# Performance work log

Hardware: AMD Instinct MI355X
Metric: run time of the kernel (lower is better)

## Reference

```python
import jax, jax.numpy as jnp
import numpy as np

K = 3          # kernel size (implied by 18/27 offset channels)
PAD = 1
STRIDE = 1


def setup_inputs() -> dict:
    key = jax.random.key(0)
    k0, k1, k2 = jax.random.split(key, 3)
    B, C, H, W = 4, 256, 64, 64
    Cout = 256
    x = jax.random.normal(k0, (B, C, H, W), jnp.float32)
    # offset/mask predicting conv: 18 offset + 9 mask channels (deform_group=1)
    w_off = jax.random.normal(k1, (27, C, K, K), jnp.float32) * 0.01
    b_off = jnp.zeros((27,), jnp.float32)
    # main deformable conv weight (bias=False)
    w = jax.random.normal(k2, (Cout, C, K, K), jnp.float32) * 0.05
    return {"x": x, "w_off": w_off, "b_off": b_off, "w": w}


def _modulated_dcn(x, w_off, b_off, w):
    B, C, H, W = x.shape
    KK = K * K
    # regular conv predicting offsets (+ mask)
    om = jax.lax.conv_general_dilated(
        x, w_off, (STRIDE, STRIDE), [(PAD, PAD), (PAD, PAD)],
        dimension_numbers=("NCHW", "OIHW", "NCHW")) + b_off[None, :, None, None]
    Ho, Wo = om.shape[2], om.shape[3]
    # channel layout: interleaved (dy, dx) per kernel tap, then 9 mask channels
    off = om[:, :2 * KK].reshape(B, KK, 2, Ho, Wo)
    mask = jax.nn.sigmoid(om[:, 2 * KK:3 * KK])            # (B, KK, Ho, Wo)

    ky, kx = jnp.meshgrid(jnp.arange(K), jnp.arange(K), indexing="ij")
    base_y = (jnp.arange(Ho) * STRIDE - PAD)[:, None]       # (Ho, 1)
    base_x = (jnp.arange(Wo) * STRIDE - PAD)[None, :]       # (1, Wo)
    # sampling positions p = p0 + pn + offset, shape (B, KK, Ho, Wo)
    py = base_y[None, None] + ky.reshape(KK)[None, :, None, None] + off[:, :, 0]
    px = base_x[None, None] + kx.reshape(KK)[None, :, None, None] + off[:, :, 1]

    y0f = jnp.floor(py)
    x0f = jnp.floor(px)
    ly = py - y0f
    lx = px - x0f
    y0 = y0f.astype(jnp.int32)
    x0 = x0f.astype(jnp.int32)

    xf = x.reshape(B, C, H * W)

    def samp(yi, xi):
        valid = ((yi >= 0) & (yi < H) & (xi >= 0) & (xi < W)).astype(x.dtype)
        idx = jnp.clip(yi, 0, H - 1) * W + jnp.clip(xi, 0, W - 1)
        v = jnp.take_along_axis(xf, idx.reshape(B, 1, -1), axis=2)
        return v.reshape(B, C, KK, Ho, Wo) * valid[:, None]

    # bilinear interpolation with zero padding outside the image
    v = (samp(y0,     x0    ) * ((1 - ly) * (1 - lx))[:, None]
         + samp(y0,     x0 + 1) * ((1 - ly) * lx)[:, None]
         + samp(y0 + 1, x0    ) * (ly * (1 - lx))[:, None]
         + samp(y0 + 1, x0 + 1) * (ly * lx)[:, None])
    v = v * mask[:, None]                                   # modulation
    # conv as contraction over (Cin, KK)
    return jnp.einsum("bckhw,ock->bohw", v, w.reshape(w.shape[0], C, KK))


def reference(x, w_off, b_off, w):
    return _modulated_dcn(x, w_off, b_off, w)
```

## Files before the change

kernel.cpp:

```cpp
#include <hip/hip_runtime.h>
#include <math.h>

#define HH 64
#define WW 64
#define CIN 256
#define COUT 256
#define KKT 9
#define HWSZ 4096
#define VP 260

typedef __bf16  v8bf   __attribute__((ext_vector_type(8)));
typedef float   v4f    __attribute__((ext_vector_type(4)));
typedef short   short8 __attribute__((ext_vector_type(8)));
typedef unsigned short ushort4v __attribute__((ext_vector_type(4)));

__device__ inline unsigned short f2bf(float f) {
    union { float f; unsigned u; } uf; uf.f = f;
    unsigned r = uf.u + 0x7fff + ((uf.u >> 16) & 1);
    return (unsigned short)(r >> 16);
}
__device__ inline float bf2f(unsigned short u) {
    union { unsigned u; float f; } uf; uf.u = ((unsigned)u) << 16;
    return uf.f;
}

__global__ __launch_bounds__(256) void k_prep(const float* __restrict__ x,
                                              const float* __restrict__ w,
                                              const float* __restrict__ w_off,
                                              unsigned short* __restrict__ x_t,
                                              unsigned short* __restrict__ wprep,
                                              unsigned short* __restrict__ woffp) {
    __shared__ float s_w[2304];
    int id  = blockIdx.x;
    int tid = threadIdx.x;
    if (id < 256) {
        int b  = id >> 6;
        int h  = id & 63;
        int px  = tid & 63;
        int oct = tid >> 6;
        const float* xr = x + (((size_t)b * CIN) * HH + h) * WW;
        unsigned short* orow = x_t + (((size_t)id) * WW + px) * CIN;
        for (int g = 0; g < 8; g++) {
            int cb = g * 32 + oct * 8;
            unsigned short v[8];
#pragma unroll
            for (int j = 0; j < 8; j++)
                v[j] = f2bf(xr[(size_t)(cb + j) * HWSZ + px]);
            *(short8*)(orow + cb) = *(short8*)v;
        }
    } else if (id < 512) {
        int o = id - 256;
        for (int i = tid; i < 2304; i += 256) s_w[i] = w[(size_t)o * 2304 + i];
        __syncthreads();
        for (int u = tid; u < 576; u += 256) {
            int t  = u >> 3;
            int kq = u & 7;
            unsigned short v[4];
#pragma unroll
            for (int j = 0; j < 4; j++) {
                int kp = t * 32 + kq * 4 + j;
                int kk = kp >> 8;
                int c  = kp & 255;
                v[j] = f2bf(s_w[c * 9 + kk]);
            }
            *(ushort4v*)&wprep[((size_t)(t * 256 + o)) * 32 + kq * 4] = *(ushort4v*)v;
        }
    } else {
        int t = id - 512;
#pragma unroll
        for (int i = 0; i < 4; i++) {
            int idx = i * 256 + tid;
            int och = idx >> 5;
            int ki  = idx & 31;
            int kp  = t * 32 + ki;
            int kk  = kp >> 8;
            int c   = kp & 255;
            float v = (och < 27) ? w_off[((size_t)och * 256 + c) * 9 + kk] : 0.f;
            woffp[(size_t)t * 1024 + idx] = f2bf(v);
        }
    }
}

__global__ __launch_bounds__(256) void k_off_mfma(const unsigned short* __restrict__ x_t,
                                                  const unsigned short* __restrict__ woffp,
                                                  const float* __restrict__ b_off,
                                                  float* __restrict__ om) {
    int id    = blockIdx.x;
    int g     = id & 7;
    int phalf = (id >> 3) & 1;
    int hi    = (id >> 4) & 7;
    int b     = id >> 7;
    int h     = g * 8 + hi;
    int p0    = phalf * 32;
    int tid  = threadIdx.x;
    int lane = tid & 63;
    int wv   = tid >> 6;
    int g2   = wv >> 1;
    int ntw  = wv & 1;
    int m16  = lane & 15;
    int quad = lane >> 4;

    __shared__ unsigned short s_row[3 * 34 * VP];
    __shared__ float s_red[2][32][33];

    const unsigned short* xb = x_t + (size_t)b * HWSZ * CIN;

    for (int u = tid; u < 3 * 1088; u += 256) {
        int row = u / 1088;
        int rem = u - row * 1088;
        int px  = rem >> 5;
        int c8  = (rem & 31) * 8;
        int y   = h + row - 1;
        int xg  = p0 + px - 1;
        short8 val = (short8)0;
        if ((unsigned)y < HH && (unsigned)xg < WW)
            val = *(const short8*)(xb + ((size_t)y * WW + xg) * CIN + c8);
        *(short8*)&s_row[(row * 34 + px) * VP + c8] = val;
    }
    __syncthreads();

    v4f acc[2];
    acc[0] = (v4f)(0.f);
    acc[1] = (v4f)(0.f);

#pragma unroll
    for (int ky = 0; ky < 3; ky++) {
#pragma unroll
        for (int kx = 0; kx < 3; kx++) {
#pragma unroll
            for (int c2 = 0; c2 < 4; c2++) {
                int ch = c2 * 2 + g2;
                int t  = (ky * 3 + kx) * 8 + ch;
                const unsigned short* wp = woffp + (size_t)t * 1024;
                short8 af0 = *(const short8*)(wp + m16 * 32 + quad * 8);
                short8 af1 = *(const short8*)(wp + (16 + m16) * 32 + quad * 8);
                short8 bfr = *(const short8*)
                    &s_row[(ky * 34 + ntw * 16 + m16 + kx) * VP + ch * 32 + quad * 8];
                acc[0] = __builtin_amdgcn_mfma_f32_16x16x32_bf16(
                    __builtin_bit_cast(v8bf, af0), __builtin_bit_cast(v8bf, bfr), acc[0], 0, 0, 0);
                acc[1] = __builtin_amdgcn_mfma_f32_16x16x32_bf16(
                    __builtin_bit_cast(v8bf, af1), __builtin_bit_cast(v8bf, bfr), acc[1], 0, 0, 0);
            }
        }
    }

#pragma unroll
    for (int mt = 0; mt < 2; mt++)
#pragma unroll
        for (int r = 0; r < 4; r++)
            s_red[g2][mt * 16 + quad * 4 + r][ntw * 16 + m16] = acc[mt][r];
    __syncthreads();

    for (int i2 = tid; i2 < 27 * 32; i2 += 256) {
        int och = i2 >> 5;
        int px  = i2 & 31;
        float s = s_red[0][och][px] + s_red[1][och][px] + b_off[och];
        om[((size_t)b * 27 + och) * HWSZ + h * WW + p0 + px] = s;
    }
}

__global__ __launch_bounds__(512, 4) void k_main(const unsigned short* __restrict__ x_t,
                                                 const float* __restrict__ om,
                                                 const unsigned short* __restrict__ wprep,
                                                 float* __restrict__ out) {
    int id    = blockIdx.x;
    int g     = id & 7;
    int phalf = (id >> 3) & 1;
    int hi    = (id >> 4) & 7;
    int b     = id >> 7;
    int h     = g * 8 + hi;
    int p0    = phalf * 32;
    int tid  = threadIdx.x;
    int lane = tid & 63;
    int oct  = tid >> 6;
    int m16  = lane & 15;
    int quad = lane >> 4;

    __shared__ int4   s_base[KKT][32];
    __shared__ float4 s_wt  [KKT][32];
    __shared__ unsigned short s_v[32 * VP];

    const float* omb = om + (size_t)b * 27 * HWSZ + h * WW;
    for (int i = tid; i < KKT * 32; i += 512) {
        int kk = i >> 5;
        int pl = i & 31;
        int p  = p0 + pl;
        float offy = omb[(size_t)(2 * kk)     * HWSZ + p];
        float offx = omb[(size_t)(2 * kk + 1) * HWSZ + p];
        float mv   = omb[(size_t)(18 + kk)    * HWSZ + p];
        int ky = kk / 3, kx = kk - 3 * (kk / 3);
        float py = (float)(h - 1 + ky) + offy;
        float px = (float)(p - 1 + kx) + offx;
        float y0f = floorf(py);
        float x0f = floorf(px);
        float ly = py - y0f, lx = px - x0f;
        int y0 = (int)y0f, x0 = (int)x0f;
        float m = 1.f / (1.f + __expf(-mv));
        bool yv0 = (unsigned)y0       < HH;
        bool yv1 = (unsigned)(y0 + 1) < HH;
        bool xv0 = (unsigned)x0       < WW;
        bool xv1 = (unsigned)(x0 + 1) < WW;
        int y0c = min(max(y0, 0), HH - 1);
        int y1c = min(max(y0 + 1, 0), HH - 1);
        int x0c = min(max(x0, 0), WW - 1);
        int x1c = min(max(x0 + 1, 0), WW - 1);
        s_base[kk][pl] = make_int4((y0c * WW + x0c) * CIN, (y0c * WW + x1c) * CIN,
                                   (y1c * WW + x0c) * CIN, (y1c * WW + x1c) * CIN);
        s_wt[kk][pl] = make_float4(
            (yv0 && xv0) ? (1.f - ly) * (1.f - lx) * m : 0.f,
            (yv0 && xv1) ? (1.f - ly) * lx         * m : 0.f,
            (yv1 && xv0) ? ly * (1.f - lx)         * m : 0.f,
            (yv1 && xv1) ? ly * lx                 * m : 0.f);
    }
    __syncthreads();

    v4f acc[2][2];
#pragma unroll
    for (int mt = 0; mt < 2; mt++)
#pragma unroll
        for (int nt = 0; nt < 2; nt++) acc[mt][nt] = (v4f)(0.f);

    const unsigned short* xb = x_t + (size_t)b * HWSZ * CIN;
    const unsigned short* xc = xb + lane * 4;

    for (int kk = 0; kk < KKT; kk++) {
#pragma unroll
        for (int i = 0; i < 4; i++) {
            int pl = oct * 4 + i;
            int4   bp = s_base[kk][pl];
            float4 wt = s_wt[kk][pl];
            ushort4v t0 = *(const ushort4v*)(xc + bp.x);
            ushort4v t1 = *(const ushort4v*)(xc + bp.y);
            ushort4v t2 = *(const ushort4v*)(xc + bp.z);
            ushort4v t3 = *(const ushort4v*)(xc + bp.w);
            unsigned short vv[4];
#pragma unroll
            for (int j = 0; j < 4; j++) {
                float val = wt.x * bf2f(t0[j]) + wt.y * bf2f(t1[j])
                          + wt.z * bf2f(t2[j]) + wt.w * bf2f(t3[j]);
                vv[j] = f2bf(val);
            }
            *(ushort4v*)&s_v[pl * VP + lane * 4] = *(ushort4v*)vv;
        }
        __syncthreads();

#pragma unroll 2
        for (int ch = 0; ch < 8; ch++) {
            int t = kk * 8 + ch;
            const unsigned short* wp = wprep + ((size_t)t * 256 + oct * 32) * 32;
            short8 af0 = *(const short8*)(wp + m16 * 32 + quad * 8);
            short8 af1 = *(const short8*)(wp + (16 + m16) * 32 + quad * 8);
            short8 bfr[2];
#pragma unroll
            for (int nt = 0; nt < 2; nt++)
                bfr[nt] = *(const short8*)&s_v[(nt * 16 + m16) * VP + ch * 32 + quad * 8];
#pragma unroll
            for (int nt = 0; nt < 2; nt++) {
                acc[0][nt] = __builtin_amdgcn_mfma_f32_16x16x32_bf16(
                    __builtin_bit_cast(v8bf, af0), __builtin_bit_cast(v8bf, bfr[nt]),
                    acc[0][nt], 0, 0, 0);
                acc[1][nt] = __builtin_amdgcn_mfma_f32_16x16x32_bf16(
                    __builtin_bit_cast(v8bf, af1), __builtin_bit_cast(v8bf, bfr[nt]),
                    acc[1][nt], 0, 0, 0);
            }
        }
        __syncthreads();
    }

    float* ob = out + ((size_t)b * COUT) * HWSZ + h * WW + p0;
#pragma unroll
    for (int mt = 0; mt < 2; mt++)
#pragma unroll
        for (int nt = 0; nt < 2; nt++)
#pragma unroll
            for (int r = 0; r < 4; r++) {
                int o = oct * 32 + mt * 16 + quad * 4 + r;
                ob[(size_t)o * HWSZ + nt * 16 + m16] = acc[mt][nt][r];
            }
}

extern "C" void kernel_launch(void* const* d_in, const int* in_sizes, int n_in,
                              void* d_out, int out_size, void* d_ws, size_t ws_size,
                              hipStream_t stream) {
    const float* x     = (const float*)d_in[0];
    const float* w_off = (const float*)d_in[1];
    const float* b_off = (const float*)d_in[2];
    const float* w     = (const float*)d_in[3];
    float* out = (float*)d_out;

    float* om = (float*)d_ws;
    unsigned short* x_t   = (unsigned short*)(om + 442368);
    unsigned short* wprep = x_t + (size_t)4 * HWSZ * CIN;
    unsigned short* woffp = wprep + 589824;

    hipLaunchKernelGGL(k_prep,     dim3(584), dim3(256), 0, stream, x, w, w_off, x_t, wprep, woffp);
    hipLaunchKernelGGL(k_off_mfma, dim3(512), dim3(256), 0, stream, x_t, woffp, b_off, om);
    hipLaunchKernelGGL(k_main,     dim3(512), dim3(512), 0, stream, x_t, om, wprep, out);
}
```

Measured before the change: 145.7 us.

## Fuse offset conv into main kernel and double-buffer the gathered tile

Removes the separate offset/mask convolution kernel. Each main-kernel block now stages the 3-row halo of x in LDS and computes its own 27 offset/mask channels with MFMA, so the om buffer no longer makes a round trip through global memory and one launch goes away. The bilinear gather loop also double-buffers the sampled tile in LDS and prefetches the next tap's four corner loads into registers, which leaves one barrier per tap instead of two. In exchange the block uses much more LDS for the halo region, which may cut blocks per CU below the launch-bounds target, and it holds more registers for the prefetched corners.

```diff
diff --git a/kernel.cpp b/kernel.cpp
--- a/kernel.cpp
+++ b/kernel.cpp
@@ -81,87 +81,10 @@
     }
 }
 
-__global__ __launch_bounds__(256) void k_off_mfma(const unsigned short* __restrict__ x_t,
-                                                  const unsigned short* __restrict__ woffp,
-                                                  const float* __restrict__ b_off,
-                                                  float* __restrict__ om) {
-    int id    = blockIdx.x;
-    int g     = id & 7;
-    int phalf = (id >> 3) & 1;
-    int hi    = (id >> 4) & 7;
-    int b     = id >> 7;
-    int h     = g * 8 + hi;
-    int p0    = phalf * 32;
-    int tid  = threadIdx.x;
-    int lane = tid & 63;
-    int wv   = tid >> 6;
-    int g2   = wv >> 1;
-    int ntw  = wv & 1;
-    int m16  = lane & 15;
-    int quad = lane >> 4;
-
-    __shared__ unsigned short s_row[3 * 34 * VP];
-    __shared__ float s_red[2][32][33];
-
-    const unsigned short* xb = x_t + (size_t)b * HWSZ * CIN;
-
-    for (int u = tid; u < 3 * 1088; u += 256) {
-        int row = u / 1088;
-        int rem = u - row * 1088;
-        int px  = rem >> 5;
-        int c8  = (rem & 31) * 8;
-        int y   = h + row - 1;
-        int xg  = p0 + px - 1;
-        short8 val = (short8)0;
-        if ((unsigned)y < HH && (unsigned)xg < WW)
-            val = *(const short8*)(xb + ((size_t)y * WW + xg) * CIN + c8);
-        *(short8*)&s_row[(row * 34 + px) * VP + c8] = val;
-    }
-    __syncthreads();
-
-    v4f acc[2];
-    acc[0] = (v4f)(0.f);
-    acc[1] = (v4f)(0.f);
-
-#pragma unroll
-    for (int ky = 0; ky < 3; ky++) {
-#pragma unroll
-        for (int kx = 0; kx < 3; kx++) {
-#pragma unroll
-            for (int c2 = 0; c2 < 4; c2++) {
-                int ch = c2 * 2 + g2;
-                int t  = (ky * 3 + kx) * 8 + ch;
-                const unsigned short* wp = woffp + (size_t)t * 1024;
-                short8 af0 = *(const short8*)(wp + m16 * 32 + quad * 8);
-                short8 af1 = *(const short8*)(wp + (16 + m16) * 32 + quad * 8);
-                short8 bfr = *(const short8*)
-                    &s_row[(ky * 34 + ntw * 16 + m16 + kx) * VP + ch * 32 + quad * 8];
-                acc[0] = __builtin_amdgcn_mfma_f32_16x16x32_bf16(
-                    __builtin_bit_cast(v8bf, af0), __builtin_bit_cast(v8bf, bfr), acc[0], 0, 0, 0);
-                acc[1] = __builtin_amdgcn_mfma_f32_16x16x32_bf16(
-                    __builtin_bit_cast(v8bf, af1), __builtin_bit_cast(v8bf, bfr), acc[1], 0, 0, 0);
-            }
-        }
-    }
-
-#pragma unroll
-    for (int mt = 0; mt < 2; mt++)
-#pragma unroll
-        for (int r = 0; r < 4; r++)
-            s_red[g2][mt * 16 + quad * 4 + r][ntw * 16 + m16] = acc[mt][r];
-    __syncthreads();
-
-    for (int i2 = tid; i2 < 27 * 32; i2 += 256) {
-        int och = i2 >> 5;
-        int px  = i2 & 31;
-        float s = s_red[0][och][px] + s_red[1][och][px] + b_off[och];
-        om[((size_t)b * 27 + och) * HWSZ + h * WW + p0 + px] = s;
-    }
-}
-
 __global__ __launch_bounds__(512, 4) void k_main(const unsigned short* __restrict__ x_t,
-                                                 const float* __restrict__ om,
                                                  const unsigned short* __restrict__ wprep,
+                                                 const unsigned short* __restrict__ woffp,
+                                                 const float* __restrict__ b_off,
                                                  float* __restrict__ out) {
     int id    = blockIdx.x;
     int g     = id & 7;
@@ -176,18 +99,77 @@
     int m16  = lane & 15;
     int quad = lane >> 4;
 
+    __shared__ __align__(16) unsigned short s_reg[3 * 34 * VP];
     __shared__ int4   s_base[KKT][32];
     __shared__ float4 s_wt  [KKT][32];
-    __shared__ unsigned short s_v[32 * VP];
-
-    const float* omb = om + (size_t)b * 27 * HWSZ + h * WW;
+    __shared__ float  s_om  [27][33];
+
+    const unsigned short* xb = x_t + (size_t)b * HWSZ * CIN;
+
+    for (int u = tid; u < 3 * 1088; u += 512) {
+        int row = u / 1088;
+        int rem = u - row * 1088;
+        int px  = rem >> 5;
+        int c8  = (rem & 31) * 8;
+        int y   = h + row - 1;
+        int xg  = p0 + px - 1;
+        short8 val = (short8)0;
+        if ((unsigned)y < HH && (unsigned)xg < WW)
+            val = *(const short8*)(xb + ((size_t)y * WW + xg) * CIN + c8);
+        *(short8*)&s_reg[(row * 34 + px) * VP + c8] = val;
+    }
+    __syncthreads();
+
+    {
+        int g2  = oct >> 1;
+        int ntw = oct & 1;
+        v4f oa[2];
+        oa[0] = (v4f)(0.f);
+        oa[1] = (v4f)(0.f);
+#pragma unroll
+        for (int ky = 0; ky < 3; ky++)
+#pragma unroll
+        for (int kx = 0; kx < 3; kx++)
+#pragma unroll
+        for (int c2 = 0; c2 < 2; c2++) {
+            int ch = c2 * 4 + g2;
+            int t  = (ky * 3 + kx) * 8 + ch;
+            const unsigned short* wp = woffp + (size_t)t * 1024;
+            short8 af0 = *(const short8*)(wp + m16 * 32 + quad * 8);
+            short8 af1 = *(const short8*)(wp + (16 + m16) * 32 + quad * 8);
+            short8 bfr = *(const short8*)
+                &s_reg[(ky * 34 + ntw * 16 + m16 + kx) * VP + ch * 32 + quad * 8];
+            oa[0] = __builtin_amdgcn_mfma_f32_16x16x32_bf16(
+                __builtin_bit_cast(v8bf, af0), __builtin_bit_cast(v8bf, bfr), oa[0], 0, 0, 0);
+            oa[1] = __builtin_amdgcn_mfma_f32_16x16x32_bf16(
+                __builtin_bit_cast(v8bf, af1), __builtin_bit_cast(v8bf, bfr), oa[1], 0, 0, 0);
+        }
+        __syncthreads();
+        float* s_red = (float*)s_reg;
+#pragma unroll
+        for (int mt = 0; mt < 2; mt++)
+#pragma unroll
+            for (int r = 0; r < 4; r++)
+                s_red[(g2 * 32 + mt * 16 + quad * 4 + r) * 33 + ntw * 16 + m16] = oa[mt][r];
+        __syncthreads();
+        for (int i2 = tid; i2 < 27 * 32; i2 += 512) {
+            int och = i2 >> 5;
+            int px  = i2 & 31;
+            float s = s_red[och * 33 + px]         + s_red[(32 + och) * 33 + px]
+                    + s_red[(64 + och) * 33 + px]  + s_red[(96 + och) * 33 + px]
+                    + b_off[och];
+            s_om[och][px] = s;
+        }
+        __syncthreads();
+    }
+
     for (int i = tid; i < KKT * 32; i += 512) {
         int kk = i >> 5;
         int pl = i & 31;
         int p  = p0 + pl;
-        float offy = omb[(size_t)(2 * kk)     * HWSZ + p];
-        float offx = omb[(size_t)(2 * kk + 1) * HWSZ + p];
-        float mv   = omb[(size_t)(18 + kk)    * HWSZ + p];
+        float offy = s_om[2 * kk][pl];
+        float offx = s_om[2 * kk + 1][pl];
+        float mv   = s_om[18 + kk][pl];
         int ky = kk / 3, kx = kk - 3 * (kk / 3);
         float py = (float)(h - 1 + ky) + offy;
         float px = (float)(p - 1 + kx) + offx;
@@ -220,29 +202,50 @@
 #pragma unroll
         for (int nt = 0; nt < 2; nt++) acc[mt][nt] = (v4f)(0.f);
 
-    const unsigned short* xb = x_t + (size_t)b * HWSZ * CIN;
     const unsigned short* xc = xb + lane * 4;
 
+    ushort4v tt[4][4];
+#pragma unroll
+    for (int i = 0; i < 4; i++) {
+        int4 bp = s_base[0][oct * 4 + i];
+        tt[i][0] = *(const ushort4v*)(xc + bp.x);
+        tt[i][1] = *(const ushort4v*)(xc + bp.y);
+        tt[i][2] = *(const ushort4v*)(xc + bp.z);
+        tt[i][3] = *(const ushort4v*)(xc + bp.w);
+    }
+
+#pragma unroll
     for (int kk = 0; kk < KKT; kk++) {
+        unsigned short* sv = s_reg + (kk & 1) * (32 * VP);
+
 #pragma unroll
         for (int i = 0; i < 4; i++) {
             int pl = oct * 4 + i;
-            int4   bp = s_base[kk][pl];
             float4 wt = s_wt[kk][pl];
-            ushort4v t0 = *(const ushort4v*)(xc + bp.x);
-            ushort4v t1 = *(const ushort4v*)(xc + bp.y);
-            ushort4v t2 = *(const ushort4v*)(xc + bp.z);
-            ushort4v t3 = *(const ushort4v*)(xc + bp.w);
             unsigned short vv[4];
 #pragma unroll
             for (int j = 0; j < 4; j++) {
-                float val = wt.x * bf2f(t0[j]) + wt.y * bf2f(t1[j])
-                          + wt.z * bf2f(t2[j]) + wt.w * bf2f(t3[j]);
+                float val = wt.x * bf2f(tt[i][0][j]) + wt.y * bf2f(tt[i][1][j])
+                          + wt.z * bf2f(tt[i][2][j]) + wt.w * bf2f(tt[i][3][j]);
                 vv[j] = f2bf(val);
             }
-            *(ushort4v*)&s_v[pl * VP + lane * 4] = *(ushort4v*)vv;
-        }
-        __syncthreads();
+            *(ushort4v*)&sv[pl * VP + lane * 4] = *(ushort4v*)vv;
+        }
+
+        if (kk < KKT - 1) {
+#pragma unroll
+            for (int i = 0; i < 4; i++) {
+                int4 bp = s_base[kk + 1][oct * 4 + i];
+                tt[i][0] = *(const ushort4v*)(xc + bp.x);
+                tt[i][1] = *(const ushort4v*)(xc + bp.y);
+                tt[i][2] = *(const ushort4v*)(xc + bp.z);
+                tt[i][3] = *(const ushort4v*)(xc + bp.w);
+            }
+        }
+
+        asm volatile("s_waitcnt lgkmcnt(0)" ::: "memory");
+        __builtin_amdgcn_s_barrier();
+        __builtin_amdgcn_sched_barrier(0);
 
 #pragma unroll 2
         for (int ch = 0; ch < 8; ch++) {
@@ -253,7 +256,7 @@
             short8 bfr[2];
 #pragma unroll
             for (int nt = 0; nt < 2; nt++)
-                bfr[nt] = *(const short8*)&s_v[(nt * 16 + m16) * VP + ch * 32 + quad * 8];
+                bfr[nt] = *(const short8*)&sv[(nt * 16 + m16) * VP + ch * 32 + quad * 8];
 #pragma unroll
             for (int nt = 0; nt < 2; nt++) {
                 acc[0][nt] = __builtin_amdgcn_mfma_f32_16x16x32_bf16(
@@ -264,7 +267,6 @@
                     acc[1][nt], 0, 0, 0);
             }
         }
-        __syncthreads();
     }
 
     float* ob = out + ((size_t)b * COUT) * HWSZ + h * WW + p0;
@@ -288,12 +290,10 @@
     const float* w     = (const float*)d_in[3];
     float* out = (float*)d_out;
 
-    float* om = (float*)d_ws;
-    unsigned short* x_t   = (unsigned short*)(om + 442368);
+    unsigned short* x_t   = (unsigned short*)d_ws;
     unsigned short* wprep = x_t + (size_t)4 * HWSZ * CIN;
     unsigned short* woffp = wprep + 589824;
 
-    hipLaunchKernelGGL(k_prep,     dim3(584), dim3(256), 0, stream, x, w, w_off, x_t, wprep, woffp);
-    hipLaunchKernelGGL(k_off_mfma, dim3(512), dim3(256), 0, stream, x_t, woffp, b_off, om);
-    hipLaunchKernelGGL(k_main,     dim3(512), dim3(512), 0, stream, x_t, om, wprep, out);
-}
+    hipLaunchKernelGGL(k_prep, dim3(584), dim3(256), 0, stream, x, w, w_off, x_t, wprep, woffp);
+    hipLaunchKernelGGL(k_main, dim3(512), dim3(512), 0, stream, x_t, wprep, woffp, b_off, out);
+}
```

Result: slower. 168.8 us (+15.9%).

## Transpose x via shared memory in prep and halve main-kernel pixel tile

Applied to the files above, without the earlier changes.

The prep kernel now converts and transposes x through a padded shared-memory tile, reading coalesced float4 rows and writing 16-byte channel vectors, with twice as many blocks. The main kernel processes 16 pixels per block instead of 32, doubling the grid to 1024 blocks and raising the launch-bounds occupancy hint. This spreads work across more CUs and waves, at the cost of reloading the weight fragments twice as often per output and doing fewer MFMAs per load.

```diff
diff --git a/kernel.cpp b/kernel.cpp
--- a/kernel.cpp
+++ b/kernel.cpp
@@ -8,6 +8,7 @@
 #define KKT 9
 #define HWSZ 4096
 #define VP 260
+#define TP 264
 
 typedef __bf16  v8bf   __attribute__((ext_vector_type(8)));
 typedef float   v4f    __attribute__((ext_vector_type(4)));
@@ -30,26 +31,38 @@
                                               unsigned short* __restrict__ x_t,
                                               unsigned short* __restrict__ wprep,
                                               unsigned short* __restrict__ woffp) {
-    __shared__ float s_w[2304];
+    __shared__ __align__(16) unsigned short s_t[32 * TP];
     int id  = blockIdx.x;
     int tid = threadIdx.x;
-    if (id < 256) {
-        int b  = id >> 6;
-        int h  = id & 63;
-        int px  = tid & 63;
-        int oct = tid >> 6;
-        const float* xr = x + (((size_t)b * CIN) * HH + h) * WW;
-        unsigned short* orow = x_t + (((size_t)id) * WW + px) * CIN;
-        for (int g = 0; g < 8; g++) {
-            int cb = g * 32 + oct * 8;
-            unsigned short v[8];
-#pragma unroll
-            for (int j = 0; j < 8; j++)
-                v[j] = f2bf(xr[(size_t)(cb + j) * HWSZ + px]);
-            *(short8*)(orow + cb) = *(short8*)v;
-        }
-    } else if (id < 512) {
-        int o = id - 256;
+    if (id < 512) {
+        int b    = id >> 7;
+        int r    = id & 127;
+        int h    = r >> 1;
+        int half = r & 1;
+        const float* xr = x + ((size_t)b * CIN) * HWSZ + h * WW + half * 32;
+#pragma unroll
+        for (int it = 0; it < 8; it++) {
+            int idx = it * 256 + tid;
+            int c   = idx >> 3;
+            int p4  = idx & 7;
+            float4 v = *(const float4*)(xr + (size_t)c * HWSZ + p4 * 4);
+            s_t[(p4 * 4 + 0) * TP + c] = f2bf(v.x);
+            s_t[(p4 * 4 + 1) * TP + c] = f2bf(v.y);
+            s_t[(p4 * 4 + 2) * TP + c] = f2bf(v.z);
+            s_t[(p4 * 4 + 3) * TP + c] = f2bf(v.w);
+        }
+        __syncthreads();
+        unsigned short* orow = x_t + (((size_t)(b * 64 + h)) * WW + half * 32) * CIN;
+#pragma unroll
+        for (int it = 0; it < 4; it++) {
+            int idx = it * 256 + tid;
+            int px  = idx >> 5;
+            int c8  = (idx & 31) * 8;
+            *(short8*)(orow + (size_t)px * CIN + c8) = *(const short8*)&s_t[px * TP + c8];
+        }
+    } else if (id < 768) {
+        float* s_w = (float*)s_t;
+        int o = id - 512;
         for (int i = tid; i < 2304; i += 256) s_w[i] = w[(size_t)o * 2304 + i];
         __syncthreads();
         for (int u = tid; u < 576; u += 256) {
@@ -66,7 +79,7 @@
             *(ushort4v*)&wprep[((size_t)(t * 256 + o)) * 32 + kq * 4] = *(ushort4v*)v;
         }
     } else {
-        int t = id - 512;
+        int t = id - 768;
 #pragma unroll
         for (int i = 0; i < 4; i++) {
             int idx = i * 256 + tid;
@@ -159,31 +172,31 @@
     }
 }
 
-__global__ __launch_bounds__(512, 4) void k_main(const unsigned short* __restrict__ x_t,
+__global__ __launch_bounds__(512, 8) void k_main(const unsigned short* __restrict__ x_t,
                                                  const float* __restrict__ om,
                                                  const unsigned short* __restrict__ wprep,
                                                  float* __restrict__ out) {
-    int id    = blockIdx.x;
-    int g     = id & 7;
-    int phalf = (id >> 3) & 1;
-    int hi    = (id >> 4) & 7;
-    int b     = id >> 7;
-    int h     = g * 8 + hi;
-    int p0    = phalf * 32;
+    int id = blockIdx.x;
+    int g  = id & 7;
+    int pq = (id >> 3) & 3;
+    int hi = (id >> 5) & 7;
+    int b  = id >> 8;
+    int h  = g * 8 + hi;
+    int p0 = pq * 16;
     int tid  = threadIdx.x;
     int lane = tid & 63;
     int oct  = tid >> 6;
     int m16  = lane & 15;
     int quad = lane >> 4;
 
-    __shared__ int4   s_base[KKT][32];
-    __shared__ float4 s_wt  [KKT][32];
-    __shared__ unsigned short s_v[32 * VP];
+    __shared__ int4   s_base[KKT][16];
+    __shared__ float4 s_wt  [KKT][16];
+    __shared__ __align__(16) unsigned short s_v[16 * VP];
 
     const float* omb = om + (size_t)b * 27 * HWSZ + h * WW;
-    for (int i = tid; i < KKT * 32; i += 512) {
-        int kk = i >> 5;
-        int pl = i & 31;
+    for (int i = tid; i < KKT * 16; i += 512) {
+        int kk = i >> 4;
+        int pl = i & 15;
         int p  = p0 + pl;
         float offy = omb[(size_t)(2 * kk)     * HWSZ + p];
         float offx = omb[(size_t)(2 * kk + 1) * HWSZ + p];
@@ -214,19 +227,17 @@
     }
     __syncthreads();
 
-    v4f acc[2][2];
-#pragma unroll
-    for (int mt = 0; mt < 2; mt++)
-#pragma unroll
-        for (int nt = 0; nt < 2; nt++) acc[mt][nt] = (v4f)(0.f);
+    v4f acc[2];
+    acc[0] = (v4f)(0.f);
+    acc[1] = (v4f)(0.f);
 
     const unsigned short* xb = x_t + (size_t)b * HWSZ * CIN;
     const unsigned short* xc = xb + lane * 4;
 
     for (int kk = 0; kk < KKT; kk++) {
 #pragma unroll
-        for (int i = 0; i < 4; i++) {
-            int pl = oct * 4 + i;
+        for (int i = 0; i < 2; i++) {
+            int pl = oct * 2 + i;
             int4   bp = s_base[kk][pl];
             float4 wt = s_wt[kk][pl];
             ushort4v t0 = *(const ushort4v*)(xc + bp.x);
@@ -250,19 +261,11 @@
             const unsigned short* wp = wprep + ((size_t)t * 256 + oct * 32) * 32;
             short8 af0 = *(const short8*)(wp + m16 * 32 + quad * 8);
             short8 af1 = *(const short8*)(wp + (16 + m16) * 32 + quad * 8);
-            short8 bfr[2];
-#pragma unroll
-            for (int nt = 0; nt < 2; nt++)
-                bfr[nt] = *(const short8*)&s_v[(nt * 16 + m16) * VP + ch * 32 + quad * 8];
-#pragma unroll
-            for (int nt = 0; nt < 2; nt++) {
-                acc[0][nt] = __builtin_amdgcn_mfma_f32_16x16x32_bf16(
-                    __builtin_bit_cast(v8bf, af0), __builtin_bit_cast(v8bf, bfr[nt]),
-                    acc[0][nt], 0, 0, 0);
-                acc[1][nt] = __builtin_amdgcn_mfma_f32_16x16x32_bf16(
-                    __builtin_bit_cast(v8bf, af1), __builtin_bit_cast(v8bf, bfr[nt]),
-                    acc[1][nt], 0, 0, 0);
-            }
+            short8 bfr = *(const short8*)&s_v[m16 * VP + ch * 32 + quad * 8];
+            acc[0] = __builtin_amdgcn_mfma_f32_16x16x32_bf16(
+                __builtin_bit_cast(v8bf, af0), __builtin_bit_cast(v8bf, bfr), acc[0], 0, 0, 0);
+            acc[1] = __builtin_amdgcn_mfma_f32_16x16x32_bf16(
+                __builtin_bit_cast(v8bf, af1), __builtin_bit_cast(v8bf, bfr), acc[1], 0, 0, 0);
         }
         __syncthreads();
     }
@@ -271,12 +274,10 @@
 #pragma unroll
     for (int mt = 0; mt < 2; mt++)
 #pragma unroll
-        for (int nt = 0; nt < 2; nt++)
-#pragma unroll
-            for (int r = 0; r < 4; r++) {
-                int o = oct * 32 + mt * 16 + quad * 4 + r;
-                ob[(size_t)o * HWSZ + nt * 16 + m16] = acc[mt][nt][r];
-            }
+        for (int r = 0; r < 4; r++) {
+            int o = oct * 32 + mt * 16 + quad * 4 + r;
+            ob[(size_t)o * HWSZ + m16] = acc[mt][r];
+        }
 }
 
 extern "C" void kernel_launch(void* const* d_in, const int* in_sizes, int n_in,
@@ -293,7 +294,7 @@
     unsigned short* wprep = x_t + (size_t)4 * HWSZ * CIN;
     unsigned short* woffp = wprep + 589824;
 
-    hipLaunchKernelGGL(k_prep,     dim3(584), dim3(256), 0, stream, x, w, w_off, x_t, wprep, woffp);
-    hipLaunchKernelGGL(k_off_mfma, dim3(512), dim3(256), 0, stream, x_t, woffp, b_off, om);
-    hipLaunchKernelGGL(k_main,     dim3(512), dim3(512), 0, stream, x_t, om, wprep, out);
-}
+    hipLaunchKernelGGL(k_prep,     dim3(840),  dim3(256), 0, stream, x, w, w_off, x_t, wprep, woffp);
+    hipLaunchKernelGGL(k_off_mfma, dim3(512),  dim3(256), 0, stream, x_t, woffp, b_off, om);
+    hipLaunchKernelGGL(k_main,     dim3(1024), dim3(512), 0, stream, x_t, om, wprep, out);
+}
```

Measured after the change: 177.6 us. 21.9% more time.
